# Optimization experiments

Hardware: AMD Instinct MI355X
Metric: run time of the kernel (lower is better)

## Reference

```python
import jax, jax.numpy as jnp
import numpy as np

B, S, E = 2, 2048, 2048
NH, NKV, HD = 32, 8, 64
GS = NH // NKV  # group size = 4
EPS = 1e-6
ROPE_THETA = 10000.0


def setup_inputs() -> dict:
    key = jax.random.key(0)
    ks = jax.random.split(key, 6)
    x = jax.random.normal(ks[0], (B, S, E), jnp.float32)
    position_ids = jnp.broadcast_to(jnp.arange(S, dtype=jnp.int32), (B, S))
    # causal additive mask [1,1,S,S]
    causal = jnp.tril(jnp.ones((S, S), jnp.bool_))
    attn_mask = jnp.where(causal, 0.0, -1e9).astype(jnp.float32)[None, None]
    sc = 0.02
    Wq = jax.random.normal(ks[1], (E, NH * HD), jnp.float32) * sc
    Wk = jax.random.normal(ks[2], (E, NKV * HD), jnp.float32) * sc
    Wv = jax.random.normal(ks[3], (E, NKV * HD), jnp.float32) * sc
    Wo = jax.random.normal(ks[4], (NH * HD, E), jnp.float32) * sc
    q_norm_w = jnp.ones((HD,), jnp.float32)
    k_norm_w = jnp.ones((HD,), jnp.float32)
    return {"x": x, "position_ids": position_ids, "attn_mask": attn_mask,
            "Wq": Wq, "Wk": Wk, "Wv": Wv, "Wo": Wo,
            "q_norm_w": q_norm_w, "k_norm_w": k_norm_w}


def rms_norm(x, w):
    dt = x.dtype
    xf = x.astype(jnp.float32)
    xf = xf * jax.lax.rsqrt(jnp.mean(xf * xf, axis=-1, keepdims=True) + EPS)
    return w * xf.astype(dt)


def apply_rope(x, position_ids):
    # x: [B, H, S, D]; rotate-half RoPE
    D = x.shape[-1]
    inv_freq = 1.0 / (ROPE_THETA ** (jnp.arange(0, D, 2, dtype=jnp.float32) / D))
    freqs = position_ids.astype(jnp.float32)[:, :, None] * inv_freq  # [B,S,D/2]
    cos = jnp.cos(freqs)[:, None]  # [B,1,S,D/2]
    sin = jnp.sin(freqs)[:, None]
    x1, x2 = x[..., : D // 2], x[..., D // 2 :]
    return jnp.concatenate([x1 * cos - x2 * sin, x2 * cos + x1 * sin], axis=-1).astype(x.dtype)


def reference(x, position_ids, attn_mask, Wq, Wk, Wv, Wo, q_norm_w, k_norm_w):
    b, s, _ = x.shape
    Q = (x @ Wq).reshape(b, s, NH, HD).transpose(0, 2, 1, 3)   # [B,NH,S,D]
    K = (x @ Wk).reshape(b, s, NKV, HD).transpose(0, 2, 1, 3)  # [B,NKV,S,D]
    V = (x @ Wv).reshape(b, s, NKV, HD).transpose(0, 2, 1, 3)
    Q = rms_norm(Q, q_norm_w)
    K = rms_norm(K, k_norm_w)
    Q = apply_rope(Q, position_ids)
    K = apply_rope(K, position_ids)
    new_kv_cache = (K, V)
    # GQA: head h attends with kv group h // GS == reshape heads -> (NKV, GS)
    Qg = Q.reshape(b, NKV, GS, s, HD)
    scores = jnp.einsum('bgqsd,bgtd->bgqst', Qg, K) / np.float32(np.sqrt(HD))
    scores = scores + attn_mask[:, :, None]  # broadcast over group dim
    attn = jax.nn.softmax(scores.astype(jnp.float32), axis=-1).astype(x.dtype)
    ctx = jnp.einsum('bgqst,bgtd->bgqsd', attn, V)             # [B,NKV,GS,S,D]
    ctx = ctx.reshape(b, NH, s, HD).transpose(0, 2, 1, 3).reshape(b, s, NH * HD)
    output = ctx @ Wo
    return output, new_kv_cache
```

## Files before the change

### kernel.cpp

```cpp
#include <hip/hip_runtime.h>
#include <stdint.h>

#define S_LEN 2048
#define EMB 2048
#define NHEADS 32
#define NKVH 8
#define HDIM 64

typedef float f32x4 __attribute__((ext_vector_type(4)));
typedef float f32x16 __attribute__((ext_vector_type(16)));
typedef __bf16 bf16x8 __attribute__((ext_vector_type(8)));
typedef unsigned int u32x4 __attribute__((ext_vector_type(4)));

typedef const __attribute__((address_space(1))) void* as1cv;
typedef __attribute__((address_space(3))) void* as3v;

__device__ __forceinline__ void gload_lds16(const void* g, void* l) {
  as1cv gp = (as1cv)(uintptr_t)g;
  as3v lp = (as3v)(uintptr_t)l;
  __builtin_amdgcn_global_load_lds(gp, lp, 16, 0, 0);
}

__device__ __forceinline__ unsigned cvt_pk_bf16(float lo, float hi) {
  unsigned r;
  asm("v_cvt_pk_bf16_f32 %0, %1, %2" : "=v"(r) : "v"(lo), "v"(hi));
  return r;
}

__device__ __forceinline__ void permswap(unsigned& a, unsigned& b) {
  asm("v_permlane32_swap_b32 %0, %1" : "+v"(a), "+v"(b));
}

__device__ __forceinline__ bf16x8 pack4(unsigned a, unsigned b, unsigned c, unsigned d) {
  union { u32x4 u; bf16x8 f; } x;
  x.u = (u32x4){a, b, c, d};
  return x.f;
}

__global__ void rope_table_kernel(float* __restrict__ cosT, float* __restrict__ sinT) {
  int p = blockIdx.x;
  int i = threadIdx.x;
  if (i < 32) {
    float inv = powf(10000.0f, -(float)i / 32.0f);
    float ang = (float)p * inv;
    cosT[p * 32 + i] = cosf(ang);
    sinT[p * 32 + i] = sinf(ang);
  }
}

__global__ __launch_bounds__(256) void cast_bf16_kernel(const float* __restrict__ in,
                                                        __bf16* __restrict__ out, int n8) {
  int i = blockIdx.x * 256 + threadIdx.x;
  if (i < n8) {
    f32x4 a = *(const f32x4*)(in + (size_t)i * 8);
    f32x4 b = *(const f32x4*)(in + (size_t)i * 8 + 4);
    bf16x8 o;
    o[0] = (__bf16)a[0]; o[1] = (__bf16)a[1]; o[2] = (__bf16)a[2]; o[3] = (__bf16)a[3];
    o[4] = (__bf16)b[0]; o[5] = (__bf16)b[1]; o[6] = (__bf16)b[2]; o[7] = (__bf16)b[3];
    *(bf16x8*)(out + (size_t)i * 8) = o;
  }
}

__global__ __launch_bounds__(256) void transpose_cast_kernel(const float* __restrict__ in,
                                                             __bf16* __restrict__ out,
                                                             int R, int C) {
  __shared__ float t[64][65];
  int c0 = blockIdx.x * 64, r0 = blockIdx.y * 64;
  int tid = threadIdx.x;
#pragma unroll
  for (int i = 0; i < 16; ++i) {
    int e = i * 256 + tid;
    int rr = e >> 6, cc = e & 63;
    t[rr][cc] = in[(size_t)(r0 + rr) * C + c0 + cc];
  }
  __syncthreads();
#pragma unroll
  for (int i = 0; i < 16; ++i) {
    int e = i * 256 + tid;
    int rr = e >> 6, cc = e & 63;
    out[(size_t)(c0 + rr) * R + r0 + cc] = (__bf16)t[cc][rr];
  }
}

template <int BM, int BN, typename OUT>
__global__ __launch_bounds__(512, 1) void gemm2ph_kernel(const __bf16* __restrict__ A,
                                                         const __bf16* __restrict__ B,
                                                         OUT* __restrict__ C,
                                                         int M, int N, int K) {
  constexpr int MF = BM / 32;
  constexpr int NF = BN / 64;
  constexpr int CHA = BM / 64, CHB = BN / 64, CH = CHA + CHB;
  constexpr int ROWS = BM + BN;
  __shared__ __align__(16) __bf16 sm[2][ROWS * 64];

  const int NT = K >> 6;
  const int nt = N / BN;
  const int nwg = (M / BM) * nt;
  const int q8 = nwg >> 3;
  int wg = blockIdx.x;
  int swz = (wg & 7) * q8 + (wg >> 3);
  int bm = swz / nt, bn = swz % nt;
  size_t m0 = (size_t)bm * BM, n0 = (size_t)bn * BN;

  int tid = threadIdx.x;
  int L = tid & 63, w = tid >> 6;
  int wr = w >> 2, wc = w & 3;
  int l15 = L & 15, hi2 = L >> 4;
  int lx = (l15 & 7) << 4;
  const int cx0 = (hi2 << 4) ^ lx;
  const int cx1 = (64 + (hi2 << 4)) ^ lx;

  int srow = tid >> 3;
  int scol = ((tid & 7) ^ (srow & 7)) << 3;
  const __bf16* pA = A + (size_t)(m0 + srow) * K + scol;
  const __bf16* pB = B + (size_t)(n0 + srow) * K + scol;

  char* smb = (char*)sm;
  const int aRow = (wr * (BM / 2) + l15) * 128;
  const int bRow = (BM + wc * (BN / 4) + l15) * 128;

  f32x4 acc[MF][NF];
#pragma unroll
  for (int m = 0; m < MF; ++m)
#pragma unroll
    for (int n = 0; n < NF; ++n) acc[m][n] = (f32x4){0.f, 0.f, 0.f, 0.f};

  auto STG = [&](int buf, int c, int t) {
    const __bf16* s = (c < CHA) ? pA + (size_t)(c << 6) * K + ((size_t)t << 6)
                                : pB + (size_t)((c - CHA) << 6) * K + ((size_t)t << 6);
    gload_lds16(s, smb + buf * (ROWS * 128) + c * 8192 + tid * 16);
  };

#pragma unroll
  for (int c = 0; c < CH; ++c) STG(0, c, 0);
#pragma unroll
  for (int c = 0; c < CH; ++c) STG(1, c, 1);
  if constexpr (CH == 7) asm volatile("s_waitcnt vmcnt(7)" ::: "memory");
  else asm volatile("s_waitcnt vmcnt(6)" ::: "memory");
  __builtin_amdgcn_s_barrier();

  for (int t = 0; t < NT; ++t) {
    const char* aC = smb + (t & 1) * (ROWS * 128);
    bf16x8 af[MF][2], bf[NF][2];
#pragma unroll
    for (int n = 0; n < NF; ++n) {
      bf[n][0] = *(const bf16x8*)(aC + bRow + n * 2048 + cx0);
      bf[n][1] = *(const bf16x8*)(aC + bRow + n * 2048 + cx1);
    }
#pragma unroll
    for (int m = 0; m < MF; ++m) {
      af[m][0] = *(const bf16x8*)(aC + aRow + m * 2048 + cx0);
      af[m][1] = *(const bf16x8*)(aC + aRow + m * 2048 + cx1);
    }
    if constexpr (MF == 8) asm volatile("s_waitcnt lgkmcnt(8)" ::: "memory");
    else asm volatile("s_waitcnt lgkmcnt(4)" ::: "memory");
    __builtin_amdgcn_sched_barrier(0);
    __builtin_amdgcn_s_setprio(1);
#pragma unroll
    for (int m = 0; m < MF / 2; ++m)
#pragma unroll
      for (int n = 0; n < NF; ++n)
#pragma unroll
        for (int kk = 0; kk < 2; ++kk)
          acc[m][n] = __builtin_amdgcn_mfma_f32_16x16x32_bf16(
              kk ? af[m][1] : af[m][0], kk ? bf[n][1] : bf[n][0], acc[m][n], 0, 0, 0);
    __builtin_amdgcn_s_setprio(0);
    asm volatile("s_waitcnt lgkmcnt(0)" ::: "memory");
    __builtin_amdgcn_sched_barrier(0);
    __builtin_amdgcn_s_barrier();
    if (t + 2 < NT) {
#pragma unroll
      for (int c = 0; c < CH; ++c) STG(t & 1, c, t + 2);
    }
    __builtin_amdgcn_s_setprio(1);
#pragma unroll
    for (int m = MF / 2; m < MF; ++m)
#pragma unroll
      for (int n = 0; n < NF; ++n)
#pragma unroll
        for (int kk = 0; kk < 2; ++kk)
          acc[m][n] = __builtin_amdgcn_mfma_f32_16x16x32_bf16(
              kk ? af[m][1] : af[m][0], kk ? bf[n][1] : bf[n][0], acc[m][n], 0, 0, 0);
    __builtin_amdgcn_s_setprio(0);
    if (t + 2 < NT) {
      if constexpr (CH == 7) asm volatile("s_waitcnt vmcnt(7)" ::: "memory");
      else asm volatile("s_waitcnt vmcnt(6)" ::: "memory");
    } else if (t + 1 < NT) {
      asm volatile("s_waitcnt vmcnt(0)" ::: "memory");
    }
    __builtin_amdgcn_s_barrier();
  }

#pragma unroll
  for (int m = 0; m < MF; ++m)
#pragma unroll
    for (int n = 0; n < NF; ++n)
#pragma unroll
      for (int r = 0; r < 4; ++r)
        C[(m0 + wr * (BM / 2) + m * 16 + (hi2 << 2) + r) * (size_t)N + n0 + wc * (BN / 4) +
          n * 16 + l15] = (OUT)acc[m][n][r];
}

__global__ __launch_bounds__(256) void rmsrope_kernel(
    const __bf16* __restrict__ QKV, const int* __restrict__ pos,
    const float* __restrict__ qw, const float* __restrict__ kw,
    const float* __restrict__ cosT, const float* __restrict__ sinT,
    __bf16* __restrict__ Qatt, __bf16* __restrict__ Katt, __bf16* __restrict__ Vtatt,
    float* __restrict__ Kc, float* __restrict__ Vc) {
  int token = blockIdx.x;
  int b = token >> 11, s = token & 2047;
  int tid = threadIdx.x, lane = tid & 63, wid = tid >> 6;
  int p = pos[token];
  int i = lane & 31;
  float cs = cosT[p * 32 + i], sn = sinT[p * 32 + i];
  const __bf16* base = QKV + (size_t)token * 3072;
  float qwl = qw[lane], kwl = kw[lane];
  const float qscale = 0.18033688011112042f;

  for (int h = wid; h < NHEADS; h += 4) {
    float v = (float)base[h * 64 + lane];
    float ss = v * v;
#pragma unroll
    for (int m = 1; m < 64; m <<= 1) ss += __shfl_xor(ss, m);
    float xn = v * rsqrtf(ss * (1.0f / 64.0f) + 1e-6f) * qwl;
    float other = __shfl_xor(xn, 32);
    float o = xn * cs + ((lane < 32) ? -other * sn : other * sn);
    Qatt[((size_t)(b * NHEADS + h) * S_LEN + s) * HDIM + lane] = (__bf16)(o * qscale);
  }
  for (int g = wid; g < NKVH; g += 4) {
    float v = (float)base[2048 + g * 64 + lane];
    float ss = v * v;
#pragma unroll
    for (int m = 1; m < 64; m <<= 1) ss += __shfl_xor(ss, m);
    float xn = v * rsqrtf(ss * (1.0f / 64.0f) + 1e-6f) * kwl;
    float other = __shfl_xor(xn, 32);
    float o = xn * cs + ((lane < 32) ? -other * sn : other * sn);
    size_t kidx = ((size_t)(b * NKVH + g) * S_LEN + s) * HDIM + lane;
    Katt[kidx] = (__bf16)o;
    Kc[kidx] = o;
  }
  for (int g = wid; g < NKVH; g += 4) {
    float v = (float)base[2560 + g * 64 + lane];
    size_t vidx = ((size_t)(b * NKVH + g) * S_LEN + s) * HDIM + lane;
    Vc[vidx] = v;
    Vtatt[((size_t)(b * NKVH + g) * HDIM + lane) * S_LEN + s] = (__bf16)v;
  }
}

__global__ __launch_bounds__(256, 2) void attn_kernel(const __bf16* __restrict__ Qatt,
                                                      const __bf16* __restrict__ Katt,
                                                      const __bf16* __restrict__ Vtatt,
                                                      __bf16* __restrict__ ctx) {
  __shared__ __align__(16) __bf16 Ks[2][4096];
  __shared__ __align__(16) __bf16 Vs[2][4096];
  int bid = blockIdx.x;
  int qt, bg;
  if (bid < 256) { qt = 31 - (bid >> 4); bg = bid & 15; }
  else { qt = (bid - 256) >> 4; bg = bid & 15; }
  int b = bg >> 3, g = bg & 7;
  int tid = threadIdx.x, lane = tid & 63, w = tid >> 6;
  int l31 = lane & 31, hi = lane >> 5;
  int h = g * 4 + w;

  const __bf16* Kg = Katt + (size_t)bg * (S_LEN * HDIM);
  const __bf16* Vg = Vtatt + (size_t)bg * (HDIM * S_LEN);
  const __bf16* Qg = Qatt + ((size_t)(b * NHEADS + h) * S_LEN + qt * 64 + l31) * HDIM;

  bf16x8 qf0[4], qf1[4];
#pragma unroll
  for (int ds = 0; ds < 4; ++ds) {
    qf0[ds] = *(const bf16x8*)(Qg + ds * 16 + (hi << 3));
    qf1[ds] = *(const bf16x8*)(Qg + 32 * HDIM + ds * 16 + (hi << 3));
  }

  f32x16 acc00, acc01, acc10, acc11;
#pragma unroll
  for (int r = 0; r < 16; ++r) { acc00[r] = 0.f; acc01[r] = 0.f; acc10[r] = 0.f; acc11[r] = 0.f; }
  float l0 = 0.f, l1 = 0.f;

  int sr = tid >> 3;
  int sc = ((tid & 7) ^ (sr & 7)) << 3;
  const __bf16* Ksrc = Kg + (size_t)sr * HDIM + sc;
  const __bf16* Vsrc = Vg + (size_t)sr * S_LEN + sc;

  gload_lds16(Ksrc, &Ks[0][tid * 8]);
  gload_lds16(Ksrc + 32 * HDIM, &Ks[0][2048 + tid * 8]);
  gload_lds16(Vsrc, &Vs[0][tid * 8]);
  gload_lds16(Vsrc + (size_t)32 * S_LEN, &Vs[0][2048 + tid * 8]);
  __syncthreads();

  int rx = (l31 & 7) << 4;

  for (int t = 0; t <= qt; ++t) {
    int cur = t & 1;
    if (t < qt) {
      const __bf16* kn = Ksrc + (size_t)(t + 1) * (64 * HDIM);
      const __bf16* vn = Vsrc + (size_t)(t + 1) * 64;
      gload_lds16(kn, &Ks[cur ^ 1][tid * 8]);
      gload_lds16(kn + 32 * HDIM, &Ks[cur ^ 1][2048 + tid * 8]);
      gload_lds16(vn, &Vs[cur ^ 1][tid * 8]);
      gload_lds16(vn + (size_t)32 * S_LEN, &Vs[cur ^ 1][2048 + tid * 8]);
    }
    f32x16 s00, s01, s10, s11;
#pragma unroll
    for (int r = 0; r < 16; ++r) { s00[r] = 0.f; s01[r] = 0.f; s10[r] = 0.f; s11[r] = 0.f; }
    {
      const char* kb0 = (const char*)Ks[cur] + (size_t)l31 * 128;
      const char* kb1 = kb0 + 4096;
#pragma unroll
      for (int dstep = 0; dstep < 4; ++dstep) {
        int cb = dstep * 32 + (hi << 4);
        bf16x8 k0 = *(const bf16x8*)(kb0 + (cb ^ rx));
        bf16x8 k1 = *(const bf16x8*)(kb1 + (cb ^ rx));
        s00 = __builtin_amdgcn_mfma_f32_32x32x16_bf16(k0, qf0[dstep], s00, 0, 0, 0);
        s01 = __builtin_amdgcn_mfma_f32_32x32x16_bf16(k1, qf0[dstep], s01, 0, 0, 0);
        s10 = __builtin_amdgcn_mfma_f32_32x32x16_bf16(k0, qf1[dstep], s10, 0, 0, 0);
        s11 = __builtin_amdgcn_mfma_f32_32x32x16_bf16(k1, qf1[dstep], s11, 0, 0, 0);
      }
    }
    if (t == qt) {
#pragma unroll
      for (int r = 0; r < 16; ++r) {
        int kb = (r & 3) + 8 * (r >> 2) + (hi << 2);
        if (kb > l31) { s00[r] = -3e38f; s11[r] = -3e38f; }
        s01[r] = -3e38f;
      }
    }
#pragma unroll
    for (int r = 0; r < 16; ++r) {
      s00[r] = __builtin_amdgcn_exp2f(s00[r]);
      s01[r] = __builtin_amdgcn_exp2f(s01[r]);
      s10[r] = __builtin_amdgcn_exp2f(s10[r]);
      s11[r] = __builtin_amdgcn_exp2f(s11[r]);
    }
    {
      float a0 = 0.f, a1 = 0.f, a2 = 0.f, a3 = 0.f;
      float b0 = 0.f, b1 = 0.f, b2 = 0.f, b3 = 0.f;
#pragma unroll
      for (int r = 0; r < 16; r += 4) {
        a0 += s00[r]; a1 += s00[r + 1]; a2 += s00[r + 2]; a3 += s00[r + 3];
        a0 += s01[r]; a1 += s01[r + 1]; a2 += s01[r + 2]; a3 += s01[r + 3];
        b0 += s10[r]; b1 += s10[r + 1]; b2 += s10[r + 2]; b3 += s10[r + 3];
        b0 += s11[r]; b1 += s11[r + 1]; b2 += s11[r + 2]; b3 += s11[r + 3];
      }
      l0 += (a0 + a1) + (a2 + a3);
      l1 += (b0 + b1) + (b2 + b3);
    }
    bf16x8 pf0[4], pf1[4];
    {
      unsigned wd[8];
#pragma unroll
      for (int i = 0; i < 8; ++i) wd[i] = cvt_pk_bf16(s00[2 * i], s00[2 * i + 1]);
      permswap(wd[0], wd[2]); permswap(wd[1], wd[3]);
      permswap(wd[4], wd[6]); permswap(wd[5], wd[7]);
      pf0[0] = pack4(wd[0], wd[1], wd[2], wd[3]);
      pf0[1] = pack4(wd[4], wd[5], wd[6], wd[7]);
#pragma unroll
      for (int i = 0; i < 8; ++i) wd[i] = cvt_pk_bf16(s01[2 * i], s01[2 * i + 1]);
      permswap(wd[0], wd[2]); permswap(wd[1], wd[3]);
      permswap(wd[4], wd[6]); permswap(wd[5], wd[7]);
      pf0[2] = pack4(wd[0], wd[1], wd[2], wd[3]);
      pf0[3] = pack4(wd[4], wd[5], wd[6], wd[7]);
#pragma unroll
      for (int i = 0; i < 8; ++i) wd[i] = cvt_pk_bf16(s10[2 * i], s10[2 * i + 1]);
      permswap(wd[0], wd[2]); permswap(wd[1], wd[3]);
      permswap(wd[4], wd[6]); permswap(wd[5], wd[7]);
      pf1[0] = pack4(wd[0], wd[1], wd[2], wd[3]);
      pf1[1] = pack4(wd[4], wd[5], wd[6], wd[7]);
#pragma unroll
      for (int i = 0; i < 8; ++i) wd[i] = cvt_pk_bf16(s11[2 * i], s11[2 * i + 1]);
      permswap(wd[0], wd[2]); permswap(wd[1], wd[3]);
      permswap(wd[4], wd[6]); permswap(wd[5], wd[7]);
      pf1[2] = pack4(wd[0], wd[1], wd[2], wd[3]);
      pf1[3] = pack4(wd[4], wd[5], wd[6], wd[7]);
    }
    {
      const char* vb0 = (const char*)Vs[cur] + (size_t)l31 * 128;
      const char* vb1 = vb0 + 4096;
#pragma unroll
      for (int ks = 0; ks < 4; ++ks) {
        int cb = ks * 32 + (hi << 4);
        bf16x8 v0 = *(const bf16x8*)(vb0 + (cb ^ rx));
        bf16x8 v1 = *(const bf16x8*)(vb1 + (cb ^ rx));
        acc00 = __builtin_amdgcn_mfma_f32_32x32x16_bf16(v0, pf0[ks], acc00, 0, 0, 0);
        acc01 = __builtin_amdgcn_mfma_f32_32x32x16_bf16(v1, pf0[ks], acc01, 0, 0, 0);
        acc10 = __builtin_amdgcn_mfma_f32_32x32x16_bf16(v0, pf1[ks], acc10, 0, 0, 0);
        acc11 = __builtin_amdgcn_mfma_f32_32x32x16_bf16(v1, pf1[ks], acc11, 0, 0, 0);
      }
    }
    __syncthreads();
  }

  l0 += __shfl_xor(l0, 32);
  l1 += __shfl_xor(l1, 32);
  float inv0 = 1.f / l0, inv1 = 1.f / l1;
  size_t orow0 = ((size_t)(b * S_LEN + qt * 64 + l31)) * EMB + h * HDIM;
  size_t orow1 = orow0 + (size_t)32 * EMB;
#pragma unroll
  for (int r = 0; r < 16; r += 2) {
    int d = (r & 3) + 8 * (r >> 2) + (hi << 2);
    unsigned w00 = cvt_pk_bf16(acc00[r] * inv0, acc00[r + 1] * inv0);
    unsigned w01 = cvt_pk_bf16(acc01[r] * inv0, acc01[r + 1] * inv0);
    unsigned w10 = cvt_pk_bf16(acc10[r] * inv1, acc10[r + 1] * inv1);
    unsigned w11 = cvt_pk_bf16(acc11[r] * inv1, acc11[r + 1] * inv1);
    *(unsigned*)((char*)ctx + (orow0 + d) * 2) = w00;
    *(unsigned*)((char*)ctx + (orow0 + 32 + d) * 2) = w01;
    *(unsigned*)((char*)ctx + (orow1 + d) * 2) = w10;
    *(unsigned*)((char*)ctx + (orow1 + 32 + d) * 2) = w11;
  }
}

extern "C" void kernel_launch(void* const* d_in, const int* in_sizes, int n_in,
                              void* d_out, int out_size, void* d_ws, size_t ws_size,
                              hipStream_t stream) {
  const float* x = (const float*)d_in[0];
  const int* pos = (const int*)d_in[1];
  const float* Wq = (const float*)d_in[3];
  const float* Wk = (const float*)d_in[4];
  const float* Wv = (const float*)d_in[5];
  const float* Wo = (const float*)d_in[6];
  const float* qw = (const float*)d_in[7];
  const float* kw = (const float*)d_in[8];

  float* out = (float*)d_out;
  float* Kc = out + (size_t)2 * 2048 * 2048;
  float* Vc = Kc + (size_t)2 * 8 * 2048 * 64;

  char* ws = (char*)d_ws;
  size_t off = 0;
  auto alloc = [&](size_t bytes) {
    char* p = ws + off;
    off += (bytes + 255) & ~(size_t)255;
    return (void*)p;
  };
  __bf16* xb = (__bf16*)alloc((size_t)4096 * 2048 * 2);
  __bf16* Wcat = (__bf16*)alloc((size_t)3072 * 2048 * 2);
  __bf16* Wot = (__bf16*)alloc((size_t)2048 * 2048 * 2);
  __bf16* QKV = (__bf16*)alloc((size_t)4096 * 3072 * 2);
  __bf16* ctx = (__bf16*)alloc((size_t)4096 * 2048 * 2);
  __bf16* Qatt = (__bf16*)alloc((size_t)2 * 32 * 2048 * 64 * 2);
  __bf16* Katt = (__bf16*)alloc((size_t)2 * 8 * 2048 * 64 * 2);
  __bf16* Vtat = (__bf16*)alloc((size_t)2 * 8 * 2048 * 64 * 2);
  float* cosT = (float*)alloc((size_t)2048 * 32 * 4);
  float* sinT = (float*)alloc((size_t)2048 * 32 * 4);

  rope_table_kernel<<<2048, 64, 0, stream>>>(cosT, sinT);
  cast_bf16_kernel<<<4096, 256, 0, stream>>>(x, xb, 4096 * 2048 / 8);
  transpose_cast_kernel<<<dim3(32, 32), 256, 0, stream>>>(Wq, Wcat, 2048, 2048);
  transpose_cast_kernel<<<dim3(8, 32), 256, 0, stream>>>(Wk, Wcat + (size_t)2048 * 2048, 2048, 512);
  transpose_cast_kernel<<<dim3(8, 32), 256, 0, stream>>>(Wv, Wcat + (size_t)2560 * 2048, 2048, 512);
  transpose_cast_kernel<<<dim3(32, 32), 256, 0, stream>>>(Wo, Wot, 2048, 2048);
  gemm2ph_kernel<256, 192, __bf16><<<256, 512, 0, stream>>>(xb, Wcat, QKV, 4096, 3072, 2048);
  rmsrope_kernel<<<4096, 256, 0, stream>>>(QKV, pos, qw, kw, cosT, sinT, Qatt, Katt, Vtat, Kc, Vc);
  attn_kernel<<<512, 256, 0, stream>>>(Qatt, Katt, Vtat, ctx);
  gemm2ph_kernel<128, 256, float><<<256, 512, 0, stream>>>(ctx, Wot, out, 4096, 2048, 2048);
}
```

Measured before the change: 193.2 us.

## Replace 8-wave GEMM with 4-wave 2x2 tiling at two blocks per CU

Rewrites the GEMM kernel to use 256-thread blocks with a 2x2 wave layout and smaller tiles (128x192 for QKV, 128x128 for output projection), launched as 512 blocks with launch bounds allowing two blocks per CU. Staging is now split into 32-row chunks, with matching vmcnt thresholds. The goal is better latency hiding through two co-resident workgroups and a finer grid that balances better across CUs. The cost is smaller per-block tiles, which lower data reuse and raise global/LDS traffic per FLOP, and the LDS footprint per block must fit twice per CU.

Result: faster. 186.2 us (-3.6%).

```diff
diff --git a/kernel.cpp b/kernel.cpp
--- a/kernel.cpp
+++ b/kernel.cpp
@@ -83,14 +83,15 @@
 }
 
 template <int BM, int BN, typename OUT>
-__global__ __launch_bounds__(512, 1) void gemm2ph_kernel(const __bf16* __restrict__ A,
-                                                         const __bf16* __restrict__ B,
-                                                         OUT* __restrict__ C,
-                                                         int M, int N, int K) {
-  constexpr int MF = BM / 32;
-  constexpr int NF = BN / 64;
-  constexpr int CHA = BM / 64, CHB = BN / 64, CH = CHA + CHB;
+__global__ __launch_bounds__(256, 2) void gemm4w_kernel(const __bf16* __restrict__ A,
+                                                        const __bf16* __restrict__ B,
+                                                        OUT* __restrict__ C,
+                                                        int M, int N, int K) {
+  constexpr int MF = (BM / 2) / 16;
+  constexpr int NF = (BN / 2) / 16;
   constexpr int ROWS = BM + BN;
+  constexpr int NCALL = ROWS / 32;
+  constexpr int CHA = BM / 32;
   __shared__ __align__(16) __bf16 sm[2][ROWS * 64];
 
   const int NT = K >> 6;
@@ -104,7 +105,7 @@
 
   int tid = threadIdx.x;
   int L = tid & 63, w = tid >> 6;
-  int wr = w >> 2, wc = w & 3;
+  int wrow = w >> 1, wcol = w & 1;
   int l15 = L & 15, hi2 = L >> 4;
   int lx = (l15 & 7) << 4;
   const int cx0 = (hi2 << 4) ^ lx;
@@ -116,8 +117,8 @@
   const __bf16* pB = B + (size_t)(n0 + srow) * K + scol;
 
   char* smb = (char*)sm;
-  const int aRow = (wr * (BM / 2) + l15) * 128;
-  const int bRow = (BM + wc * (BN / 4) + l15) * 128;
+  const int aRow = (wrow * (BM / 2) + l15) * 128;
+  const int bRow = (BM + wcol * (BN / 2) + l15) * 128;
 
   f32x4 acc[MF][NF];
 #pragma unroll
@@ -126,17 +127,17 @@
     for (int n = 0; n < NF; ++n) acc[m][n] = (f32x4){0.f, 0.f, 0.f, 0.f};
 
   auto STG = [&](int buf, int c, int t) {
-    const __bf16* s = (c < CHA) ? pA + (size_t)(c << 6) * K + ((size_t)t << 6)
-                                : pB + (size_t)((c - CHA) << 6) * K + ((size_t)t << 6);
-    gload_lds16(s, smb + buf * (ROWS * 128) + c * 8192 + tid * 16);
+    const __bf16* s = (c < CHA) ? pA + (size_t)(c << 5) * K + ((size_t)t << 6)
+                                : pB + (size_t)((c - CHA) << 5) * K + ((size_t)t << 6);
+    gload_lds16(s, smb + buf * (ROWS * 128) + c * 4096 + tid * 16);
   };
 
 #pragma unroll
-  for (int c = 0; c < CH; ++c) STG(0, c, 0);
-#pragma unroll
-  for (int c = 0; c < CH; ++c) STG(1, c, 1);
-  if constexpr (CH == 7) asm volatile("s_waitcnt vmcnt(7)" ::: "memory");
-  else asm volatile("s_waitcnt vmcnt(6)" ::: "memory");
+  for (int c = 0; c < NCALL; ++c) STG(0, c, 0);
+#pragma unroll
+  for (int c = 0; c < NCALL; ++c) STG(1, c, 1);
+  if constexpr (NCALL == 10) asm volatile("s_waitcnt vmcnt(10)" ::: "memory");
+  else asm volatile("s_waitcnt vmcnt(8)" ::: "memory");
   __builtin_amdgcn_s_barrier();
 
   for (int t = 0; t < NT; ++t) {
@@ -152,8 +153,7 @@
       af[m][0] = *(const bf16x8*)(aC + aRow + m * 2048 + cx0);
       af[m][1] = *(const bf16x8*)(aC + aRow + m * 2048 + cx1);
     }
-    if constexpr (MF == 8) asm volatile("s_waitcnt lgkmcnt(8)" ::: "memory");
-    else asm volatile("s_waitcnt lgkmcnt(4)" ::: "memory");
+    asm volatile("s_waitcnt lgkmcnt(4)" ::: "memory");
     __builtin_amdgcn_sched_barrier(0);
     __builtin_amdgcn_s_setprio(1);
 #pragma unroll
@@ -170,7 +170,7 @@
     __builtin_amdgcn_s_barrier();
     if (t + 2 < NT) {
 #pragma unroll
-      for (int c = 0; c < CH; ++c) STG(t & 1, c, t + 2);
+      for (int c = 0; c < NCALL; ++c) STG(t & 1, c, t + 2);
     }
     __builtin_amdgcn_s_setprio(1);
 #pragma unroll
@@ -183,8 +183,8 @@
               kk ? af[m][1] : af[m][0], kk ? bf[n][1] : bf[n][0], acc[m][n], 0, 0, 0);
     __builtin_amdgcn_s_setprio(0);
     if (t + 2 < NT) {
-      if constexpr (CH == 7) asm volatile("s_waitcnt vmcnt(7)" ::: "memory");
-      else asm volatile("s_waitcnt vmcnt(6)" ::: "memory");
+      if constexpr (NCALL == 10) asm volatile("s_waitcnt vmcnt(10)" ::: "memory");
+      else asm volatile("s_waitcnt vmcnt(8)" ::: "memory");
     } else if (t + 1 < NT) {
       asm volatile("s_waitcnt vmcnt(0)" ::: "memory");
     }
@@ -197,8 +197,8 @@
     for (int n = 0; n < NF; ++n)
 #pragma unroll
       for (int r = 0; r < 4; ++r)
-        C[(m0 + wr * (BM / 2) + m * 16 + (hi2 << 2) + r) * (size_t)N + n0 + wc * (BN / 4) +
-          n * 16 + l15] = (OUT)acc[m][n][r];
+        C[(m0 + wrow * (BM / 2) + m * 16 + (hi2 << 2) + r) * (size_t)N + n0 +
+          wcol * (BN / 2) + n * 16 + l15] = (OUT)acc[m][n][r];
 }
 
 __global__ __launch_bounds__(256) void rmsrope_kernel(
@@ -450,8 +450,8 @@
   transpose_cast_kernel<<<dim3(8, 32), 256, 0, stream>>>(Wk, Wcat + (size_t)2048 * 2048, 2048, 512);
   transpose_cast_kernel<<<dim3(8, 32), 256, 0, stream>>>(Wv, Wcat + (size_t)2560 * 2048, 2048, 512);
   transpose_cast_kernel<<<dim3(32, 32), 256, 0, stream>>>(Wo, Wot, 2048, 2048);
-  gemm2ph_kernel<256, 192, __bf16><<<256, 512, 0, stream>>>(xb, Wcat, QKV, 4096, 3072, 2048);
+  gemm4w_kernel<128, 192, __bf16><<<512, 256, 0, stream>>>(xb, Wcat, QKV, 4096, 3072, 2048);
   rmsrope_kernel<<<4096, 256, 0, stream>>>(QKV, pos, qw, kw, cosT, sinT, Qatt, Katt, Vtat, Kc, Vc);
   attn_kernel<<<512, 256, 0, stream>>>(Qatt, Katt, Vtat, ctx);
-  gemm2ph_kernel<128, 256, float><<<256, 512, 0, stream>>>(ctx, Wot, out, 4096, 2048, 2048);
-}
+  gemm4w_kernel<128, 128, float><<<512, 256, 0, stream>>>(ctx, Wot, out, 4096, 2048, 2048);
+}
```
